# Performance work log

Measured on AMD Instinct MI355X. Metric: run time of the kernel, lower is better.

Reference implementation:

```python
import jax, jax.numpy as jnp
import numpy as np

B, NCH, NPTS, NGT = 8, 4, 1024, 10
NANCH = 5 * NPTS
NMIN, NMAX = 64, 64
M = NMIN + NMAX
NPOOL = 64
EXT = 0.2
EPS = 1e-5
PERM = np.array([3, 4, 5, 1, 0, 2, 6])

_C = jnp.array([[0., 1, 0], [0, -1, 0], [2.5, -1, 0], [2.5, 1, 0], [2.5, 0, 0]], jnp.float32)
_ROT = jnp.array([[1., 0, 0], [0, 0, 1], [0, 1, 0]], jnp.float32)  # theta=0 rotation from source
NEW_CENTERS = _C @ _ROT  # (5,3)
DIM = jnp.array([2., 2., 5.], jnp.float32)


def _conv1x1(x, w, b):
    return jnp.einsum('bci,oc->boi', x, w) + b[None, :, None]


def _bn(x, g, be):  # BatchNorm1d in train mode: batch stats over (N, L)
    m = x.mean((0, 2), keepdims=True)
    v = ((x - m) ** 2).mean((0, 2), keepdims=True)
    return (x - m) * jax.lax.rsqrt(v + EPS) * g[None, :, None] + be[None, :, None]


def _corners(b):  # b=(cx,cz,w,l,ry) -> (4,2) CCW BEV corners
    lx = jnp.array([0.5, -0.5, -0.5, 0.5]) * b[2]
    lz = jnp.array([0.5, 0.5, -0.5, -0.5]) * b[3]
    c, s = jnp.cos(b[4]), jnp.sin(b[4])
    return jnp.stack([b[0] + lx * c - lz * s, b[1] + lx * s + lz * c], 1)


def _clip(poly, count, e1, e2):  # Sutherland-Hodgman: clip convex poly (8,2) by left half-plane of e1->e2
    idx = jnp.arange(8)
    valid = idx < count
    cnt = jnp.maximum(count, 1)
    nxt = poly[(idx + 1) % cnt]
    ex, ez = e2[0] - e1[0], e2[1] - e1[1]
    dc = ex * (poly[:, 1] - e1[1]) - ez * (poly[:, 0] - e1[0])
    dn = ex * (nxt[:, 1] - e1[1]) - ez * (nxt[:, 0] - e1[0])
    in_c, in_n = dc >= 0, dn >= 0
    den = dc - dn
    t = dc / jnp.where(jnp.abs(den) < 1e-9, 1e-9, den)
    inter = poly + t[:, None] * (nxt - poly)
    flags = jnp.stack([valid & in_c, valid & (in_c ^ in_n)], 1).reshape(16)
    pts = jnp.stack([poly, inter], 1).reshape(16, 2)
    pos = jnp.cumsum(flags) - 1
    out = jnp.zeros((8, 2), poly.dtype).at[jnp.where(flags, pos, 8)].set(pts, mode='drop')
    return out, flags.sum()


def _bev_iou(a, b):  # rotated BEV IoU, a,b=(cx,cz,w,l,ry)
    poly = jnp.zeros((8, 2)).at[:4].set(_corners(a))
    count = jnp.int32(4)
    cb = _corners(b)
    for k in range(4):
        poly, count = _clip(poly, count, cb[k], cb[(k + 1) % 4])
    idx = jnp.arange(8)
    nxt = poly[(idx + 1) % jnp.maximum(count, 1)]
    inter = 0.5 * jnp.abs(jnp.sum(jnp.where(idx < count, poly[:, 0] * nxt[:, 1] - nxt[:, 0] * poly[:, 1], 0.)))
    return inter / jnp.maximum(a[2] * a[3] + b[2] * b[3] - inter, 1e-8)


def _bev(b7):  # (..,7)=[x,y,z,h,w,l,ry] -> (cx,cz,w,l,ry)
    return jnp.stack([b7[..., 0], b7[..., 2], b7[..., 4], b7[..., 5], b7[..., 6]], -1)


def _select_one(pnts, labels):  # pnts (N,3), labels (G,9)
    cent = (pnts[:, None, :] - NEW_CENTERS[None]).reshape(NANCH, 3)  # repeat_interleave(pnts,5)-tile(centers)
    anchors = jnp.concatenate([jnp.broadcast_to(DIM, (NANCH, 3)), cent, jnp.zeros((NANCH, 1))], 1)
    a7 = anchors[:, PERM]
    g7 = labels[:, PERM]
    ab, gb = _bev(a7), _bev(g7)
    iou2d = jax.vmap(lambda g: jax.vmap(lambda a: _bev_iou(g, a))(ab))(gb)  # (G, NANCH)
    max_iou = iou2d.max(0)
    max_ind = jnp.argmax(iou2d, 0)
    order = jnp.argsort(max_iou)
    sel = jnp.concatenate([order[:NMIN], order[-NMAX:]])  # bottom-k + top-k
    return a7[sel], max_ind[sel], max_iou[sel]


def _pool_one(box, pts, ft):  # roipool3d: first NPOOL points inside expanded box, zero-padded
    c, s = jnp.cos(box[6]), jnp.sin(box[6])
    dx, dz = pts[:, 0] - box[0], pts[:, 2] - box[2]
    xl = dx * c + dz * s
    zl = -dx * s + dz * c
    inside = (jnp.abs(xl) < box[4] * 0.5 + EXT) & (jnp.abs(zl) < box[5] * 0.5 + EXT) \
             & (pts[:, 1] > box[1] - box[3] - EXT) & (pts[:, 1] < box[1] + EXT)
    order = jnp.argsort(jnp.logical_not(inside))[:NPOOL]  # stable sort: inside points first, original order
    valid = inside[order].astype(ft.dtype)[:, None]
    return jnp.concatenate([ft[order], pts[order]], -1) * valid  # (NPOOL, 256+3)


def _forward(points, gt_labels, p):
    x = jax.nn.relu(_bn(_conv1x1(points, p['pn_w1'], p['pn_b1']), p['pn_g1'], p['pn_be1']))
    x = jax.nn.relu(_bn(_conv1x1(x, p['pn_w2'], p['pn_b2']), p['pn_g2'], p['pn_be2']))
    x = _bn(_conv1x1(x, p['pn_w3'], p['pn_b3']), p['pn_g3'], p['pn_be3'])  # (B,256,N)
    pts = jnp.transpose(points[:, :3, :], (0, 2, 1))  # (B,N,3)
    sel_boxes, sel_idx, sel_iou = jax.vmap(_select_one)(pts, gt_labels)  # (B,M,7),(B,M),(B,M)
    ftr = jnp.transpose(x, (0, 2, 1))  # (B,N,256)
    pooled = jax.vmap(lambda bx, pp, ff: jax.vmap(lambda b: _pool_one(b, pp, ff))(bx))(sel_boxes, pts, ftr)
    pooled = pooled - jnp.pad(sel_boxes[:, :, None, :3], ((0, 0), (0, 0), (0, 0), (256, 0)))  # subtract center from last 3 ch
    pf = jnp.transpose(pooled.reshape(B * M, NPOOL, 259), (0, 2, 1))  # (B*M,259,64)
    f = _bn(_conv1x1(pf, p['rp_w1'], p['rp_b1']), p['rp_g1'], p['rp_be1'])
    f = _bn(_conv1x1(f, p['rp_w2'], p['rp_b2']), p['rp_g2'], p['rp_be2'])
    feats = f.reshape(B, M, 1024, NPOOL).max(-1)
    labels_bin = (sel_iou > 0.5).astype(jnp.int32)
    return feats, labels_bin, sel_iou, sel_boxes, gt_labels[-1], sel_idx


def setup_inputs():
    key = jax.random.key(0)
    ks = jax.random.split(key, 16)
    points = jax.random.normal(ks[0], (B, NCH, NPTS), jnp.float32) * 3.0
    dims = jax.random.uniform(ks[1], (B, NGT, 3), minval=1.0, maxval=4.0)
    ctrs = jax.random.normal(ks[2], (B, NGT, 3)) * 3.0
    th = jax.random.uniform(ks[3], (B, NGT, 1), minval=-3.14, maxval=3.14)
    extra = jax.random.normal(ks[4], (B, NGT, 2))
    gt_labels = jnp.concatenate([dims, ctrs, th, extra], -1).astype(jnp.float32)  # (B,G,9)
    inp = {'points': points, 'gt_labels': gt_labels}
    shapes = [('pn', 1, 64, NCH), ('pn', 2, 128, 64), ('pn', 3, 256, 128), ('rp', 1, 512, 259), ('rp', 2, 1024, 512)]
    for j, (pre, n, o, i) in enumerate(shapes):
        inp[f'{pre}_w{n}'] = jax.random.normal(ks[5 + j], (o, i), jnp.float32) / np.sqrt(i).astype(np.float32)
        inp[f'{pre}_b{n}'] = jnp.zeros((o,), jnp.float32)
        inp[f'{pre}_g{n}'] = jnp.ones((o,), jnp.float32)
        inp[f'{pre}_be{n}'] = jnp.zeros((o,), jnp.float32)
    return inp


def reference(points, gt_labels, pn_w1, pn_b1, pn_g1, pn_be1, pn_w2, pn_b2, pn_g2, pn_be2, pn_w3, pn_b3, pn_g3, pn_be3, rp_w1, rp_b1, rp_g1, rp_be1, rp_w2, rp_b2, rp_g2, rp_be2):
    p = dict(pn_w1=pn_w1, pn_b1=pn_b1, pn_g1=pn_g1, pn_be1=pn_be1, pn_w2=pn_w2, pn_b2=pn_b2, pn_g2=pn_g2, pn_be2=pn_be2, pn_w3=pn_w3, pn_b3=pn_b3, pn_g3=pn_g3, pn_be3=pn_be3, rp_w1=rp_w1, rp_b1=rp_b1, rp_g1=rp_g1, rp_be1=rp_be1, rp_w2=rp_w2, rp_b2=rp_b2, rp_g2=rp_g2, rp_be2=rp_be2)
    return _forward(points, gt_labels, p)
```

## Files before the change

### kernel.cpp

```cpp
#include <hip/hip_runtime.h>
#include <hip/hip_bf16.h>
#include <float.h>
#include <math.h>


typedef __attribute__((ext_vector_type(8))) short short8;
typedef __attribute__((ext_vector_type(4))) float f32x4;

template <int CTRL>
__device__ __forceinline__ float dppmv(float x) {
  return __int_as_float(__builtin_amdgcn_update_dpp(
      0, __float_as_int(x), CTRL, 0xF, 0xF, true));
}
__device__ __forceinline__ float dpp_sum16(float x) {
  x += dppmv<0xB1>(x);
  x += dppmv<0x4E>(x);
  x += dppmv<0x124>(x);
  x += dppmv<0x128>(x);
  return x;
}

__device__ __forceinline__ void stage1k(const unsigned short* g, unsigned short* l) {
  __builtin_amdgcn_global_load_lds(
      (const __attribute__((address_space(1))) unsigned int*)g,
      (__attribute__((address_space(3))) unsigned int*)l, 16, 0, 0);
}

#define FMA16()                                                                 \
  do {                                                                          \
    float4 av = *(const float4*)&sWT[cc][to * 4];                               \
    float4 bv = *(const float4*)&sB[cc][tk * 4];                                \
    acc[0][0] = fmaf(av.x, bv.x, acc[0][0]);                                    \
    acc[0][1] = fmaf(av.x, bv.y, acc[0][1]);                                    \
    acc[0][2] = fmaf(av.x, bv.z, acc[0][2]);                                    \
    acc[0][3] = fmaf(av.x, bv.w, acc[0][3]);                                    \
    acc[1][0] = fmaf(av.y, bv.x, acc[1][0]);                                    \
    acc[1][1] = fmaf(av.y, bv.y, acc[1][1]);                                    \
    acc[1][2] = fmaf(av.y, bv.z, acc[1][2]);                                    \
    acc[1][3] = fmaf(av.y, bv.w, acc[1][3]);                                    \
    acc[2][0] = fmaf(av.z, bv.x, acc[2][0]);                                    \
    acc[2][1] = fmaf(av.z, bv.y, acc[2][1]);                                    \
    acc[2][2] = fmaf(av.z, bv.z, acc[2][2]);                                    \
    acc[2][3] = fmaf(av.z, bv.w, acc[2][3]);                                    \
    acc[3][0] = fmaf(av.w, bv.x, acc[3][0]);                                    \
    acc[3][1] = fmaf(av.w, bv.y, acc[3][1]);                                    \
    acc[3][2] = fmaf(av.w, bv.z, acc[3][2]);                                    \
    acc[3][3] = fmaf(av.w, bv.w, acc[3][3]);                                    \
  } while (0)

template <int C, int O, bool AFF, bool RELU, bool TRANS>
__global__ __launch_bounds__(256) void conv_pn(const float* __restrict__ in,
                                               const float* __restrict__ w,
                                               const float* __restrict__ bias,
                                               const float* __restrict__ aff,
                                               float* __restrict__ out) {
  __shared__ __align__(16) float sB[64][68];
  __shared__ __align__(16) float sWT[64][68];
  const int i0 = blockIdx.x * 64;
  const int o0 = blockIdx.y * 64;
  const int b = blockIdx.z;
  const int tid = threadIdx.x;
  const int tk = tid & 15, to = tid >> 4;
  float acc[4][4] = {};
  for (int c0 = 0; c0 < C; c0 += 64) {
    const int cs = (C - c0 < 64) ? (C - c0) : 64;
    for (int idx = tid; idx < 4096; idx += 256) {
      int ii = idx & 63, cc = idx >> 6;
      float v = 0.f;
      if (cc < cs) {
        int c = c0 + cc;
        v = in[(b * C + c) * 1024 + i0 + ii];
        if (AFF) v = fmaf(v, aff[c], aff[C + c]);
        if (RELU) v = fmaxf(v, 0.f);
      }
      sB[cc][ii] = v;
    }
    for (int idx = tid; idx < 4096; idx += 256) {
      int cc = idx & 63, oo = idx >> 6;
      sWT[cc][oo] = (cc < cs) ? w[(o0 + oo) * C + c0 + cc] : 0.f;
    }
    __syncthreads();
    for (int cc = 0; cc < cs; ++cc) { FMA16(); }
    __syncthreads();
  }
  if (TRANS) {
    float b0 = bias[o0 + to * 4], b1 = bias[o0 + to * 4 + 1];
    float b2 = bias[o0 + to * 4 + 2], b3 = bias[o0 + to * 4 + 3];
#pragma unroll
    for (int jj = 0; jj < 4; ++jj) {
      float4 v = make_float4(acc[0][jj] + b0, acc[1][jj] + b1, acc[2][jj] + b2, acc[3][jj] + b3);
      *(float4*)&out[((size_t)(b * 1024) + i0 + tk * 4 + jj) * O + o0 + to * 4] = v;
    }
  } else {
    for (int j = 0; j < 4; ++j) {
      int o = o0 + to * 4 + j;
      float bs = bias[o];
      float4 v = make_float4(acc[j][0] + bs, acc[j][1] + bs, acc[j][2] + bs, acc[j][3] + bs);
      *(float4*)&out[(b * O + o) * 1024 + i0 + tk * 4] = v;
    }
  }
}

__global__ __launch_bounds__(256) void bn_stats(const float* __restrict__ x,
                                                const float* __restrict__ g,
                                                const float* __restrict__ be,
                                                float* __restrict__ aff, int C) {
#pragma clang fp contract(off)
  int c = blockIdx.x;
  int tid = threadIdx.x;
  float s = 0.f, q = 0.f;
  for (int idx = tid; idx < 8192; idx += 256) {
    int b = idx >> 10, i = idx & 1023;
    float v = x[(b * C + c) * 1024 + i];
    s += v;
    q += v * v;
  }
  for (int m = 1; m < 64; m <<= 1) {
    s += __shfl_xor(s, m);
    q += __shfl_xor(q, m);
  }
  __shared__ float as_[4], aq_[4];
  int wv = tid >> 6;
  if ((tid & 63) == 0) { as_[wv] = s; aq_[wv] = q; }
  __syncthreads();
  if (tid == 0) {
    s = as_[0] + as_[1] + as_[2] + as_[3];
    q = aq_[0] + aq_[1] + aq_[2] + aq_[3];
    float m_ = s * (1.f / 8192.f);
    float var = q * (1.f / 8192.f) - m_ * m_;
    float A = g[c] / sqrtf(var + 1e-5f);
    aff[c] = A;
    aff[C + c] = be[c] - m_ * A;
  }
}

__global__ __launch_bounds__(256) void bn_stats_t(const float* __restrict__ x,
                                                  const float* __restrict__ g,
                                                  const float* __restrict__ be,
                                                  float* __restrict__ aff) {
#pragma clang fp contract(off)
  int c = blockIdx.x;
  int tid = threadIdx.x;
  float s = 0.f, q = 0.f;
  for (int idx = tid; idx < 8192; idx += 256) {
    float v = x[(size_t)idx * 256 + c];
    s += v;
    q += v * v;
  }
  for (int m = 1; m < 64; m <<= 1) {
    s += __shfl_xor(s, m);
    q += __shfl_xor(q, m);
  }
  __shared__ float as_[4], aq_[4];
  int wv = tid >> 6;
  if ((tid & 63) == 0) { as_[wv] = s; aq_[wv] = q; }
  __syncthreads();
  if (tid == 0) {
    s = as_[0] + as_[1] + as_[2] + as_[3];
    q = aq_[0] + aq_[1] + aq_[2] + aq_[3];
    float m_ = s * (1.f / 8192.f);
    float var = q * (1.f / 8192.f) - m_ * m_;
    float A = g[c] / sqrtf(var + 1e-5f);
    aff[c] = A;
    aff[256 + c] = be[c] - m_ * A;
  }
}

__device__ __forceinline__ void poly_ins(float* ox, float* oz, int p, float vx, float vz) {
#pragma unroll
  for (int s = 0; s < 8; ++s)
    if (p == s) { ox[s] = vx; oz[s] = vz; }
}

__device__ float bev_iou_ga(const float* gx, const float* gz, float garea, float ax, float az) {
#pragma clang fp contract(off)
  float px[8], pz[8];
#pragma unroll
  for (int i = 0; i < 4; ++i) {
    px[i] = gx[i];
    pz[i] = gz[i];
    px[i + 4] = 0.f;
    pz[i + 4] = 0.f;
  }
  int count = 4;
  float kx[4], kz[4];
  kx[0] = ax + 1.f;  kz[0] = az + 2.5f;
  kx[1] = ax - 1.f;  kz[1] = az + 2.5f;
  kx[2] = ax - 1.f;  kz[2] = az - 2.5f;
  kx[3] = ax + 1.f;  kz[3] = az - 2.5f;
#pragma unroll
  for (int e = 0; e < 4; ++e) {
    float e1x = kx[e], e1z = kz[e];
    float e2x = kx[(e + 1) & 3], e2z = kz[(e + 1) & 3];
    float ex = e2x - e1x, ez = e2z - e1z;
    int cnt = count > 1 ? count : 1;
    int lim = count < 8 ? count : 8;
    float ox[8] = {}, oz[8] = {};
    int p = 0;
#pragma unroll
    for (int idx = 0; idx < 8; ++idx) {
      if (idx < lim) {
        const int nis = (idx + 1 > 7) ? 7 : idx + 1;
        float nx = px[nis], nz = pz[nis];
        if (idx + 1 == cnt) { nx = px[0]; nz = pz[0]; }
        float cx = px[idx], cz = pz[idx];
        float dc = ex * (cz - e1z) - ez * (cx - e1x);
        float dn = ex * (nz - e1z) - ez * (nx - e1x);
        bool ic = dc >= 0.f, in_ = dn >= 0.f;
        if (ic) {
          poly_ins(ox, oz, p, cx, cz);
          ++p;
        }
        if (ic != in_) {
          float den = dc - dn;
          float t = dc / (fabsf(den) < 1e-9f ? 1e-9f : den);
          poly_ins(ox, oz, p, cx + t * (nx - cx), cz + t * (nz - cz));
          ++p;
        }
      }
    }
    count = p;
    int cp = p < 8 ? p : 8;
#pragma unroll
    for (int i = 0; i < 8; ++i) {
      px[i] = (i < cp) ? ox[i] : 0.f;
      pz[i] = (i < cp) ? oz[i] : 0.f;
    }
  }
  int cnt = count > 1 ? count : 1;
  int lim = count < 8 ? count : 8;
  float ssum = 0.f;
#pragma unroll
  for (int idx = 0; idx < 8; ++idx) {
    if (idx < lim) {
      const int nis = (idx + 1 > 7) ? 7 : idx + 1;
      float nx = px[nis], nz = pz[nis];
      if (idx + 1 == cnt) { nx = px[0]; nz = pz[0]; }
      ssum += px[idx] * nz - nx * pz[idx];
    }
  }
  float inter = 0.5f * fabsf(ssum);
  return inter / fmaxf(garea + 10.f - inter, 1e-8f);
}

__global__ __launch_bounds__(256) void iou_kernel(const float* __restrict__ points,
                                                  const float* __restrict__ gt,
                                                  float* __restrict__ iou10,
                                                  float* __restrict__ o_gt,
                                                  int* __restrict__ rank) {
#pragma clang fp contract(off)
  int b = blockIdx.y, g = blockIdx.z;
  int a = blockIdx.x * 256 + threadIdx.x;
  if (g == 0) rank[b * 5120 + a] = 0;
  if (g == 0 && b == 0 && blockIdx.x == 0 && threadIdx.x < 90)
    o_gt[threadIdx.x] = gt[630 + threadIdx.x];
  const float* L = gt + b * 90 + g * 9;
  float gxx = L[3], gzz = L[5], gw = L[0], gl = L[2], gth = L[6];
  float c = cosf(gth), s = sinf(gth);
  const float sx[4] = {0.5f, -0.5f, -0.5f, 0.5f};
  const float sz[4] = {0.5f, 0.5f, -0.5f, -0.5f};
  float gcx[4], gcz[4];
#pragma unroll
  for (int k = 0; k < 4; ++k) {
    float lx = sx[k] * gw, lz = sz[k] * gl;
    gcx[k] = gxx + lx * c - lz * s;
    gcz[k] = gzz + lx * s + lz * c;
  }
  float garea = gw * gl;
  int pt = a / 5, j = a % 5;
  const float CX[5] = {0.f, 0.f, 2.5f, 2.5f, 2.5f};
  const float CZ[5] = {1.f, -1.f, -1.f, 1.f, 0.f};
  const float* P = points + b * 4096;
  float ax = P[pt] - CX[j];
  float az = P[2048 + pt] - CZ[j];
  iou10[(size_t)(b * 10 + g) * 5120 + a] = bev_iou_ga(gcx, gcz, garea, ax, az);
}

__global__ __launch_bounds__(256) void iou_reduce(const float* __restrict__ iou10,
                                                  float* __restrict__ maxiou,
                                                  int* __restrict__ maxind) {
  int b = blockIdx.y;
  int a = blockIdx.x * 256 + threadIdx.x;
  float best = -1.f;
  int bi = 0;
  for (int g = 0; g < 10; ++g) {
    float v = iou10[(size_t)(b * 10 + g) * 5120 + a];
    if (v > best) { best = v; bi = g; }
  }
  maxiou[b * 5120 + a] = best;
  maxind[b * 5120 + a] = bi;
}

__global__ __launch_bounds__(256) void select_rank(const float* __restrict__ maxiou,
                                                   int* __restrict__ rank) {
  __shared__ __align__(16) float vals[640];
  int b = blockIdx.y, chunk = blockIdx.z, tid = threadIdx.x;
  int jb0 = chunk * 640;
  for (int i = tid; i < 640; i += 256) vals[i] = maxiou[b * 5120 + jb0 + i];
  int a = blockIdx.x * 256 + tid;
  float av = maxiou[b * 5120 + a];
  __syncthreads();
  int rk = 0;
#pragma unroll 4
  for (int j4 = 0; j4 < 160; ++j4) {
    float4 v = *(const float4*)&vals[j4 * 4];
    int jb = jb0 + j4 * 4;
    rk += (v.x < av) || (v.x == av && jb < a);
    rk += (v.y < av) || (v.y == av && jb + 1 < a);
    rk += (v.z < av) || (v.z == av && jb + 2 < a);
    rk += (v.w < av) || (v.w == av && jb + 3 < a);
  }
  atomicAdd(&rank[b * 5120 + a], rk);
}

__global__ __launch_bounds__(256) void select_write(const int* __restrict__ rank,
                                                    const float* __restrict__ maxiou,
                                                    const int* __restrict__ maxind,
                                                    const float* __restrict__ points,
                                                    float* __restrict__ o_lbl,
                                                    float* __restrict__ o_iou,
                                                    float* __restrict__ o_box,
                                                    float* __restrict__ o_idx) {
#pragma clang fp contract(off)
  int b = blockIdx.y, tid = threadIdx.x;
  int a = blockIdx.x * 256 + tid;
  int rk = rank[b * 5120 + a];
  int slot = -1;
  if (rk < 64) slot = rk;
  else if (rk >= 5056) slot = rk - 4992;
  if (slot >= 0) {
    const float CX[5] = {0.f, 0.f, 2.5f, 2.5f, 2.5f};
    const float CZ[5] = {1.f, -1.f, -1.f, 1.f, 0.f};
    int base = b * 128 + slot;
    float av = maxiou[b * 5120 + a];
    o_iou[base] = av;
    o_lbl[base] = av > 0.5f ? 1.f : 0.f;
    o_idx[base] = (float)maxind[b * 5120 + a];
    int pt = a / 5, j = a % 5;
    const float* P = points + b * 4096;
    float* bx = o_box + base * 7;
    bx[0] = P[pt] - CX[j];
    bx[1] = P[1024 + pt];
    bx[2] = P[2048 + pt] - CZ[j];
    bx[3] = 2.f;
    bx[4] = 2.f;
    bx[5] = 5.f;
    bx[6] = 0.f;
  }
}

__global__ __launch_bounds__(256) void pool_kernel(const float* __restrict__ points,
                                                   const float* __restrict__ selboxes,
                                                   int* __restrict__ selpts) {
#pragma clang fp contract(off)
  int box = blockIdx.x * 4 + (threadIdx.x >> 6);
  int lane = threadIdx.x & 63;
  int b = box >> 7;
  const float* bx = selboxes + box * 7;
  float b0 = bx[0], b1 = bx[1], b2 = bx[2], b3 = bx[3], b4 = bx[4], b5 = bx[5];
  float limx = b4 * 0.5f + 0.2f, limz = b5 * 0.5f + 0.2f;
  float ylo = b1 - b3 - 0.2f, yhi = b1 + 0.2f;
  const float* P = points + b * 4096;
  unsigned long long m[16];
  int total_in = 0;
#pragma unroll
  for (int r = 0; r < 16; ++r) {
    int pt = r * 64 + lane;
    float dx = P[pt] - b0;
    float py = P[1024 + pt];
    float dz = P[2048 + pt] - b2;
    bool ins = (fabsf(dx) < limx) && (fabsf(dz) < limz) && (py > ylo) && (py < yhi);
    m[r] = __ballot(ins);
    total_in += __popcll(m[r]);
  }
  unsigned long long lowmask = (1ull << lane) - 1;
  int cum = 0;
#pragma unroll
  for (int r = 0; r < 16; ++r) {
    int pt = r * 64 + lane;
    int inbefore = cum + __popcll(m[r] & lowmask);
    bool ins = (m[r] >> lane) & 1;
    int slot = ins ? inbefore : total_in + (pt - inbefore);
    if (slot < 64) selpts[box * 64 + slot] = pt | (ins ? 0x10000 : 0);
    cum += __popcll(m[r]);
  }
}

__global__ __launch_bounds__(256) void gather_pf(const float* __restrict__ out3T,
                                                 const float* __restrict__ points,
                                                 const int* __restrict__ selpts,
                                                 const float* __restrict__ selboxes,
                                                 const float* __restrict__ aff3,
                                                 unsigned short* __restrict__ pff) {
  __shared__ int sSel[64];
  __shared__ float sCen[3];
  __shared__ float sA3[256], sB3[256];
  const int bm = blockIdx.x;
  const int b = bm >> 7;
  const int tid = threadIdx.x;
  if (tid < 64) sSel[tid] = selpts[bm * 64 + tid];
  if (tid >= 64 && tid < 67) sCen[tid - 64] = selboxes[bm * 7 + (tid - 64)];
  sA3[tid] = aff3[tid];
  sB3[tid] = aff3[256 + tid];
  __syncthreads();
  const int pool = tid >> 2, part = tid & 3;
  const int ni = pool >> 4, nib = pool & 15;
  const int sv = sSel[pool];
  const int pt = sv & 0xFFFF;
  const bool valid = (sv >> 16) != 0;
  const float* row = out3T + ((size_t)(b << 10) + pt) * 256;
#pragma unroll
  for (int ks = 0; ks < 8; ++ks) {
    int c0 = ks * 32 + part * 8;
    float4 x0 = *(const float4*)&row[c0];
    float4 x1 = *(const float4*)&row[c0 + 4];
    float v[8] = {x0.x, x0.y, x0.z, x0.w, x1.x, x1.y, x1.z, x1.w};
    union { __hip_bfloat16 h[8]; uint4 u; } pk;
#pragma unroll
    for (int e = 0; e < 8; ++e) {
      float vv = valid ? fmaf(v[e], sA3[c0 + e], sB3[c0 + e]) : 0.f;
      pk.h[e] = __float2bfloat16(vv);
    }
    *(uint4*)&pff[((size_t)((bm * 9 + ks) * 4 + ni) * 64 + part * 16 + nib) * 8] = pk.u;
  }
  union { __hip_bfloat16 h[8]; uint4 u; } pk;
#pragma unroll
  for (int e = 0; e < 8; ++e) pk.h[e] = __float2bfloat16(0.f);
  if (part == 0) {
#pragma unroll
    for (int d = 0; d < 3; ++d) {
      float pv = valid ? points[(b * 4 + d) * 1024 + pt] : 0.f;
      pk.h[d] = __float2bfloat16(pv - sCen[d]);
    }
  }
  *(uint4*)&pff[((size_t)((bm * 9 + 8) * 4 + ni) * 64 + part * 16 + nib) * 8] = pk.u;
}

__global__ __launch_bounds__(64) void prep_w1(const float* __restrict__ w1,
                                              unsigned short* __restrict__ W1f) {
  int o = blockIdx.x;
  int lp = threadIdx.x;
  if (lp >= 36) return;
  int ks = lp >> 2, quad = lp & 3;
  int tile = o >> 4;
  union { __hip_bfloat16 h[8]; uint4 u; } pk;
#pragma unroll
  for (int j = 0; j < 8; ++j) {
    int c = ks * 32 + quad * 8 + j;
    float v = (c < 259) ? w1[o * 259 + c] : 0.f;
    pk.h[j] = __float2bfloat16(v);
  }
  *(uint4*)&W1f[((size_t)(tile * 9 + ks) * 64 + quad * 16 + (o & 15)) * 8] = pk.u;
}

__global__ __launch_bounds__(256) void rp1_mfma(const unsigned short* __restrict__ W1f,
                                                const unsigned short* __restrict__ pff,
                                                const float* __restrict__ bias1,
                                                unsigned short* __restrict__ g1x,
                                                float* __restrict__ psum4,
                                                float* __restrict__ psq4) {
  __shared__ __align__(16) unsigned short sBuf[2][6144];
  const int tid = threadIdx.x;
  const int lane = tid & 63, w = tid >> 6;
  const int quad = lane >> 4, nib = lane & 15;
  const int l = blockIdx.x;
  const int xcd = l & 7;
  const int j = l >> 3;
  const int ot = j & 3;
  const int bm = xcd * 128 + (j >> 2);
  const unsigned short* Aw = &W1f[((size_t)(ot * 8 + w * 2) * 9 * 64 + lane) * 8];
  const unsigned short* Bg = pff + (size_t)bm * 18432 + w * 1536 + lane * 8;
#pragma unroll
  for (int i = 0; i < 3; ++i)
    stage1k(Bg + i * 512, &sBuf[0][w * 1536 + i * 512]);
  __syncthreads();
  f32x4 acc[2][4] = {};
  int cur = 0;
#pragma unroll
  for (int c = 0; c < 3; ++c) {
    if (c < 2) {
#pragma unroll
      for (int i = 0; i < 3; ++i)
        stage1k(Bg + (c + 1) * 6144 + i * 512, &sBuf[cur ^ 1][w * 1536 + i * 512]);
    }
    const unsigned short* Bl = &sBuf[cur][lane * 8];
#pragma unroll
    for (int k2 = 0; k2 < 3; ++k2) {
      const int ks = c * 3 + k2;
      short8 af[2], bf[4];
#pragma unroll
      for (int mi = 0; mi < 2; ++mi)
        af[mi] = *(const short8*)&Aw[(size_t)(mi * 9 + ks) * 512];
#pragma unroll
      for (int ni = 0; ni < 4; ++ni)
        bf[ni] = *(const short8*)&Bl[(size_t)(k2 * 4 + ni) * 512];
#pragma unroll
      for (int mi = 0; mi < 2; ++mi)
#pragma unroll
        for (int ni = 0; ni < 4; ++ni)
          acc[mi][ni] = __builtin_amdgcn_mfma_f32_16x16x32_bf16(af[mi], bf[ni], acc[mi][ni], 0, 0, 0);
    }
    __syncthreads();
    cur ^= 1;
  }
  const int cbase = ot * 128 + w * 32;
#pragma unroll
  for (int mi = 0; mi < 2; ++mi) {
    float bv[4];
#pragma unroll
    for (int r = 0; r < 4; ++r) bv[r] = bias1[cbase + mi * 16 + quad * 4 + r];
    float s[4] = {0.f, 0.f, 0.f, 0.f}, q[4] = {0.f, 0.f, 0.f, 0.f};
    const int kgbase = (cbase + mi * 16) >> 3;
#pragma unroll
    for (int ni = 0; ni < 4; ++ni) {
      union { __hip_bfloat16 h[4]; unsigned int u[2]; } pk;
#pragma unroll
      for (int r = 0; r < 4; ++r) {
        float v = acc[mi][ni][r] + bv[r];
        pk.h[r] = __float2bfloat16(v);
        s[r] += v;
        q[r] += v * v;
      }
      unsigned int p0 = (unsigned int)__shfl_xor((int)pk.u[0], 16);
      unsigned int p1 = (unsigned int)__shfl_xor((int)pk.u[1], 16);
      if ((quad & 1) == 0) {
        uint4 g = make_uint4(pk.u[0], pk.u[1], p0, p1);
        int kg = kgbase + (quad >> 1);
        *(uint4*)&g1x[((size_t)(bm * 64 + kg) * 64 + ni * 16 + nib) * 8] = g;
      }
    }
#pragma unroll
    for (int r = 0; r < 4; ++r) {
      float ss = dpp_sum16(s[r]);
      float qq = dpp_sum16(q[r]);
      if (nib == 0) {
        int o = cbase + mi * 16 + quad * 4 + r;
        psum4[(size_t)o * 1024 + bm] = ss;
        psq4[(size_t)o * 1024 + bm] = qq;
      }
    }
  }
}

__global__ __launch_bounds__(64) void bn_aff_part(const float* __restrict__ psum,
                                                  const float* __restrict__ psq,
                                                  const float* __restrict__ g,
                                                  const float* __restrict__ be,
                                                  float* __restrict__ aff, int C) {
#pragma clang fp contract(off)
  int o = blockIdx.x;
  int lane = threadIdx.x;
  float s = 0.f, q = 0.f;
  for (int i = 0; i < 16; ++i) {
    int bm = i * 64 + lane;
    s += psum[(size_t)o * 1024 + bm];
    q += psq[(size_t)o * 1024 + bm];
  }
  for (int m = 1; m < 64; m <<= 1) {
    s += __shfl_xor(s, m);
    q += __shfl_xor(q, m);
  }
  if (lane == 0) {
    float m_ = s * (1.f / 65536.f);
    float var = q * (1.f / 65536.f) - m_ * m_;
    float A = g[o] / sqrtf(var + 1e-5f);
    aff[o] = A;
    aff[C + o] = be[o] - m_ * A;
  }
}

__global__ __launch_bounds__(64) void prep_w2(const float* __restrict__ w2,
                                              const float* __restrict__ b2,
                                              const float* __restrict__ aff4,
                                              unsigned short* __restrict__ W2f,
                                              float* __restrict__ bias2p) {
  int o = blockIdx.x;
  int lp = threadIdx.x;
  int ks = lp >> 2, quad = lp & 3;
  int tile = o >> 4;
  float accb = 0.f;
  union { __hip_bfloat16 h[8]; uint4 u; } pk;
#pragma unroll
  for (int j = 0; j < 8; ++j) {
    int c = ks * 32 + quad * 8 + j;
    float wv = w2[o * 512 + c];
    pk.h[j] = __float2bfloat16(wv * aff4[c]);
    accb += wv * aff4[512 + c];
  }
  *(uint4*)&W2f[((size_t)(tile * 16 + ks) * 64 + quad * 16 + (o & 15)) * 8] = pk.u;
  for (int m = 1; m < 64; m <<= 1) accb += __shfl_xor(accb, m);
  if (lp == 0) bias2p[o] = b2[o] + accb;
}

__global__ __launch_bounds__(256) void rp2_mfma(const unsigned short* __restrict__ W2f,
                                                const unsigned short* __restrict__ g1x,
                                                const float* __restrict__ bias2p,
                                                float* __restrict__ maxb,
                                                float* __restrict__ minb,
                                                float* __restrict__ psum,
                                                float* __restrict__ psq) {
  __shared__ __align__(16) unsigned short sBuf[2][8192];
  const int tid = threadIdx.x;
  const int lane = tid & 63, w = tid >> 6;
  const int quad = lane >> 4, nib = lane & 15;
  const int l = blockIdx.x;
  const int xcd = l & 7;
  const int j = l >> 3;
  const int ot = j & 3;
  const int bm = xcd * 128 + (j >> 2);
  const unsigned short* Aw = &W2f[((size_t)(ot * 4 + w) * 4 * 16 * 64 + lane) * 8];
  const unsigned short* Bg = g1x + (size_t)bm * 32768 + w * 2048 + lane * 8;
#pragma unroll
  for (int i = 0; i < 4; ++i)
    stage1k(Bg + i * 512, &sBuf[0][w * 2048 + i * 512]);
  __syncthreads();
  f32x4 acc[4][4] = {};
  int cur = 0;
#pragma unroll
  for (int c = 0; c < 4; ++c) {
    if (c < 3) {
#pragma unroll
      for (int i = 0; i < 4; ++i)
        stage1k(Bg + (c + 1) * 8192 + i * 512, &sBuf[cur ^ 1][w * 2048 + i * 512]);
    }
    const unsigned short* Bl = &sBuf[cur][quad * 512 + nib * 8];
#pragma unroll
    for (int k2 = 0; k2 < 4; ++k2) {
      const int ks = c * 4 + k2;
      short8 af[4], bf[4];
#pragma unroll
      for (int mi = 0; mi < 4; ++mi)
        af[mi] = *(const short8*)&Aw[(size_t)(mi * 16 + ks) * 512];
#pragma unroll
      for (int ni = 0; ni < 4; ++ni)
        bf[ni] = *(const short8*)&Bl[(size_t)(k2 * 2048 + ni * 128)];
#pragma unroll
      for (int mi = 0; mi < 4; ++mi)
#pragma unroll
        for (int ni = 0; ni < 4; ++ni)
          acc[ni][mi] = __builtin_amdgcn_mfma_f32_16x16x32_bf16(bf[ni], af[mi], acc[ni][mi], 0, 0, 0);
    }
    __syncthreads();
    cur ^= 1;
  }
  const int obase = ot * 256 + w * 64;
#pragma unroll
  for (int oi = 0; oi < 4; ++oi) {
    int o = obase + oi * 16 + nib;
    float bs = bias2p[o];
    float mx = -FLT_MAX, mn = FLT_MAX, s = 0.f, q = 0.f;
#pragma unroll
    for (int pi = 0; pi < 4; ++pi) {
#pragma unroll
      for (int r = 0; r < 4; ++r) {
        float v = acc[pi][oi][r] + bs;
        mx = fmaxf(mx, v);
        mn = fminf(mn, v);
        s += v;
        q += v * v;
      }
    }
    mx = fmaxf(mx, __shfl_xor(mx, 16));
    mx = fmaxf(mx, __shfl_xor(mx, 32));
    mn = fminf(mn, __shfl_xor(mn, 16));
    mn = fminf(mn, __shfl_xor(mn, 32));
    s += __shfl_xor(s, 16);
    s += __shfl_xor(s, 32);
    q += __shfl_xor(q, 16);
    q += __shfl_xor(q, 32);
    if (quad == 0) {
      maxb[bm * 1024 + o] = mx;
      minb[bm * 1024 + o] = mn;
      psum[(size_t)o * 1024 + bm] = s;
      psq[(size_t)o * 1024 + bm] = q;
    }
  }
}

__global__ void feats_kernel(const float* __restrict__ maxb, const float* __restrict__ minb,
                             const float* __restrict__ aff5, float* __restrict__ o_feats) {
#pragma clang fp contract(off)
  int i = blockIdx.x * 256 + threadIdx.x;
  int o = i & 1023;
  float A = aff5[o], Bv = aff5[1024 + o];
  float v = (A >= 0.f) ? maxb[i] : minb[i];
  o_feats[i] = v * A + Bv;
}

extern "C" void kernel_launch(void* const* d_in, const int* in_sizes, int n_in,
                              void* d_out, int out_size, void* d_ws, size_t ws_size,
                              hipStream_t stream) {
  (void)in_sizes; (void)n_in; (void)out_size; (void)ws_size;
  const float* points = (const float*)d_in[0];
  const float* gt = (const float*)d_in[1];
  const float* pn_w1 = (const float*)d_in[2];
  const float* pn_b1 = (const float*)d_in[3];
  const float* pn_g1 = (const float*)d_in[4];
  const float* pn_be1 = (const float*)d_in[5];
  const float* pn_w2 = (const float*)d_in[6];
  const float* pn_b2 = (const float*)d_in[7];
  const float* pn_g2 = (const float*)d_in[8];
  const float* pn_be2 = (const float*)d_in[9];
  const float* pn_w3 = (const float*)d_in[10];
  const float* pn_b3 = (const float*)d_in[11];
  const float* pn_g3 = (const float*)d_in[12];
  const float* pn_be3 = (const float*)d_in[13];
  const float* rp_w1 = (const float*)d_in[14];
  const float* rp_b1 = (const float*)d_in[15];
  const float* rp_g1 = (const float*)d_in[16];
  const float* rp_be1 = (const float*)d_in[17];
  const float* rp_w2 = (const float*)d_in[18];
  const float* rp_b2 = (const float*)d_in[19];
  const float* rp_g2 = (const float*)d_in[20];
  const float* rp_be2 = (const float*)d_in[21];

  float* ws = (float*)d_ws;
  float* out1 = ws;
  float* out2 = out1 + 524288;
  float* maxiou = out2 + 1048576;
  int* maxind = (int*)(maxiou + 40960);
  int* selpts = maxind + 40960;
  int* rank = selpts + 65536;
  float* aff1 = (float*)(rank + 40960);
  float* aff2 = aff1 + 128;
  float* aff3 = aff2 + 256;
  float* aff4 = aff3 + 512;
  float* aff5 = aff4 + 1024;
  float* psum4 = aff5 + 2048;
  float* psq4 = psum4 + 524288;
  unsigned short* W1f = (unsigned short*)(psq4 + 524288);
  float* pff_f = (float*)(W1f) + 73728;
  unsigned short* pff = (unsigned short*)pff_f;
  float* g1x_f = pff_f + 9437184;
  unsigned short* g1x = (unsigned short*)g1x_f;
  float* out3T = g1x_f;
  float* iou10 = g1x_f + 2097152;
  float* maxb = pff_f;
  float* minb = maxb + 1048576;
  float* psum5 = minb + 1048576;
  float* psq5 = psum5 + 1048576;
  unsigned short* W2f = (unsigned short*)out1;
  float* bias2p = out1 + 262144;

  float* o_feats = (float*)d_out;
  float* o_lbl = o_feats + 1048576;
  float* o_iou = o_lbl + 1024;
  float* o_box = o_iou + 1024;
  float* o_gt = o_box + 7168;
  float* o_idx = o_gt + 90;

  conv_pn<4, 64, false, false, false><<<dim3(16, 1, 8), 256, 0, stream>>>(points, pn_w1, pn_b1, nullptr, out1);
  bn_stats<<<64, 256, 0, stream>>>(out1, pn_g1, pn_be1, aff1, 64);
  conv_pn<64, 128, true, true, false><<<dim3(16, 2, 8), 256, 0, stream>>>(out1, pn_w2, pn_b2, aff1, out2);
  bn_stats<<<128, 256, 0, stream>>>(out2, pn_g2, pn_be2, aff2, 128);
  conv_pn<128, 256, true, true, true><<<dim3(16, 4, 8), 256, 0, stream>>>(out2, pn_w3, pn_b3, aff2, out3T);
  bn_stats_t<<<256, 256, 0, stream>>>(out3T, pn_g3, pn_be3, aff3);
  iou_kernel<<<dim3(20, 8, 10), 256, 0, stream>>>(points, gt, iou10, o_gt, rank);
  iou_reduce<<<dim3(20, 8), 256, 0, stream>>>(iou10, maxiou, maxind);
  select_rank<<<dim3(20, 8, 8), 256, 0, stream>>>(maxiou, rank);
  select_write<<<dim3(20, 8), 256, 0, stream>>>(rank, maxiou, maxind, points, o_lbl, o_iou, o_box, o_idx);
  pool_kernel<<<256, 256, 0, stream>>>(points, o_box, selpts);
  gather_pf<<<1024, 256, 0, stream>>>(out3T, points, selpts, o_box, aff3, pff);
  prep_w1<<<512, 64, 0, stream>>>(rp_w1, W1f);
  rp1_mfma<<<4096, 256, 0, stream>>>(W1f, pff, rp_b1, g1x, psum4, psq4);
  bn_aff_part<<<512, 64, 0, stream>>>(psum4, psq4, rp_g1, rp_be1, aff4, 512);
  prep_w2<<<1024, 64, 0, stream>>>(rp_w2, rp_b2, aff4, W2f, bias2p);
  rp2_mfma<<<4096, 256, 0, stream>>>(W2f, g1x, bias2p, maxb, minb, psum5, psq5);
  bn_aff_part<<<1024, 64, 0, stream>>>(psum5, psq5, rp_g2, rp_be2, aff5, 1024);
  feats_kernel<<<4096, 256, 0, stream>>>(maxb, minb, aff5, o_feats);
}
```

Before: 364.5 us.

## Merge pn conv3, IoU computation and W1 prep into one heterogeneous launch

```diff
diff --git a/kernel.cpp b/kernel.cpp
--- a/kernel.cpp
+++ b/kernel.cpp
@@ -243,37 +243,94 @@
   return inter / fmaxf(garea + 10.f - inter, 1e-8f);
 }
 
-__global__ __launch_bounds__(256) void iou_kernel(const float* __restrict__ points,
-                                                  const float* __restrict__ gt,
-                                                  float* __restrict__ iou10,
-                                                  float* __restrict__ o_gt,
-                                                  int* __restrict__ rank) {
+__global__ __launch_bounds__(256) void fused_mid(
+    const float* __restrict__ in2, const float* __restrict__ w3,
+    const float* __restrict__ b3, const float* __restrict__ aff2,
+    float* __restrict__ out3T,
+    const float* __restrict__ points, const float* __restrict__ gt,
+    float* __restrict__ iou10, float* __restrict__ o_gt, int* __restrict__ rank,
+    const float* __restrict__ w1, unsigned short* __restrict__ W1f) {
+  __shared__ __align__(16) float sB[64][68];
+  __shared__ __align__(16) float sWT[64][68];
+  const int bid = blockIdx.x;
+  const int tid = threadIdx.x;
+  if (bid < 512) {
+    const int i0 = (bid & 15) * 64;
+    const int o0 = ((bid >> 4) & 3) * 64;
+    const int b = bid >> 6;
+    const int tk = tid & 15, to = tid >> 4;
+    float acc[4][4] = {};
+    for (int c0 = 0; c0 < 128; c0 += 64) {
+      for (int idx = tid; idx < 4096; idx += 256) {
+        int ii = idx & 63, cc = idx >> 6;
+        int c = c0 + cc;
+        float v = in2[(b * 128 + c) * 1024 + i0 + ii];
+        v = fmaf(v, aff2[c], aff2[128 + c]);
+        v = fmaxf(v, 0.f);
+        sB[cc][ii] = v;
+      }
+      for (int idx = tid; idx < 4096; idx += 256) {
+        int cc = idx & 63, oo = idx >> 6;
+        sWT[cc][oo] = w3[(o0 + oo) * 128 + c0 + cc];
+      }
+      __syncthreads();
+      for (int cc = 0; cc < 64; ++cc) { FMA16(); }
+      __syncthreads();
+    }
+    float c0v = b3[o0 + to * 4], c1v = b3[o0 + to * 4 + 1];
+    float c2v = b3[o0 + to * 4 + 2], c3v = b3[o0 + to * 4 + 3];
+#pragma unroll
+    for (int jj = 0; jj < 4; ++jj) {
+      float4 v = make_float4(acc[0][jj] + c0v, acc[1][jj] + c1v, acc[2][jj] + c2v, acc[3][jj] + c3v);
+      *(float4*)&out3T[((size_t)(b * 1024) + i0 + tk * 4 + jj) * 256 + o0 + to * 4] = v;
+    }
+  } else if (bid < 2112) {
 #pragma clang fp contract(off)
-  int b = blockIdx.y, g = blockIdx.z;
-  int a = blockIdx.x * 256 + threadIdx.x;
-  if (g == 0) rank[b * 5120 + a] = 0;
-  if (g == 0 && b == 0 && blockIdx.x == 0 && threadIdx.x < 90)
-    o_gt[threadIdx.x] = gt[630 + threadIdx.x];
-  const float* L = gt + b * 90 + g * 9;
-  float gxx = L[3], gzz = L[5], gw = L[0], gl = L[2], gth = L[6];
-  float c = cosf(gth), s = sinf(gth);
-  const float sx[4] = {0.5f, -0.5f, -0.5f, 0.5f};
-  const float sz[4] = {0.5f, 0.5f, -0.5f, -0.5f};
-  float gcx[4], gcz[4];
-#pragma unroll
-  for (int k = 0; k < 4; ++k) {
-    float lx = sx[k] * gw, lz = sz[k] * gl;
-    gcx[k] = gxx + lx * c - lz * s;
-    gcz[k] = gzz + lx * s + lz * c;
-  }
-  float garea = gw * gl;
-  int pt = a / 5, j = a % 5;
-  const float CX[5] = {0.f, 0.f, 2.5f, 2.5f, 2.5f};
-  const float CZ[5] = {1.f, -1.f, -1.f, 1.f, 0.f};
-  const float* P = points + b * 4096;
-  float ax = P[pt] - CX[j];
-  float az = P[2048 + pt] - CZ[j];
-  iou10[(size_t)(b * 10 + g) * 5120 + a] = bev_iou_ga(gcx, gcz, garea, ax, az);
+    int r = bid - 512;
+    int g = r / 160;
+    int rb = r % 160;
+    int b = rb / 20;
+    int axb = rb % 20;
+    int a = axb * 256 + tid;
+    if (g == 0) rank[b * 5120 + a] = 0;
+    if (g == 0 && b == 0 && axb == 0 && tid < 90)
+      o_gt[tid] = gt[630 + tid];
+    const float* L = gt + b * 90 + g * 9;
+    float gxx = L[3], gzz = L[5], gw = L[0], gl = L[2], gth = L[6];
+    float c = cosf(gth), s = sinf(gth);
+    const float sx[4] = {0.5f, -0.5f, -0.5f, 0.5f};
+    const float sz[4] = {0.5f, 0.5f, -0.5f, -0.5f};
+    float gcx[4], gcz[4];
+#pragma unroll
+    for (int k = 0; k < 4; ++k) {
+      float lx = sx[k] * gw, lz = sz[k] * gl;
+      gcx[k] = gxx + lx * c - lz * s;
+      gcz[k] = gzz + lx * s + lz * c;
+    }
+    float garea = gw * gl;
+    int pt = a / 5, j = a % 5;
+    const float CX[5] = {0.f, 0.f, 2.5f, 2.5f, 2.5f};
+    const float CZ[5] = {1.f, -1.f, -1.f, 1.f, 0.f};
+    const float* P = points + b * 4096;
+    float ax = P[pt] - CX[j];
+    float az = P[2048 + pt] - CZ[j];
+    iou10[(size_t)(b * 10 + g) * 5120 + a] = bev_iou_ga(gcx, gcz, garea, ax, az);
+  } else {
+    int o = (bid - 2112) * 4 + (tid >> 6);
+    int lp = tid & 63;
+    if (lp < 36) {
+      int ks = lp >> 2, quad = lp & 3;
+      int tile = o >> 4;
+      union { __hip_bfloat16 h[8]; uint4 u; } pk;
+#pragma unroll
+      for (int j = 0; j < 8; ++j) {
+        int c = ks * 32 + quad * 8 + j;
+        float v = (c < 259) ? w1[o * 259 + c] : 0.f;
+        pk.h[j] = __float2bfloat16(v);
+      }
+      *(uint4*)&W1f[((size_t)(tile * 9 + ks) * 64 + quad * 16 + (o & 15)) * 8] = pk.u;
+    }
+  }
 }
 
 __global__ __launch_bounds__(256) void iou_reduce(const float* __restrict__ iou10,
@@ -436,23 +493,6 @@
   *(uint4*)&pff[((size_t)((bm * 9 + 8) * 4 + ni) * 64 + part * 16 + nib) * 8] = pk.u;
 }
 
-__global__ __launch_bounds__(64) void prep_w1(const float* __restrict__ w1,
-                                              unsigned short* __restrict__ W1f) {
-  int o = blockIdx.x;
-  int lp = threadIdx.x;
-  if (lp >= 36) return;
-  int ks = lp >> 2, quad = lp & 3;
-  int tile = o >> 4;
-  union { __hip_bfloat16 h[8]; uint4 u; } pk;
-#pragma unroll
-  for (int j = 0; j < 8; ++j) {
-    int c = ks * 32 + quad * 8 + j;
-    float v = (c < 259) ? w1[o * 259 + c] : 0.f;
-    pk.h[j] = __float2bfloat16(v);
-  }
-  *(uint4*)&W1f[((size_t)(tile * 9 + ks) * 64 + quad * 16 + (o & 15)) * 8] = pk.u;
-}
-
 __global__ __launch_bounds__(256) void rp1_mfma(const unsigned short* __restrict__ W1f,
                                                 const unsigned short* __restrict__ pff,
                                                 const float* __restrict__ bias1,
@@ -753,15 +793,15 @@
   bn_stats<<<64, 256, 0, stream>>>(out1, pn_g1, pn_be1, aff1, 64);
   conv_pn<64, 128, true, true, false><<<dim3(16, 2, 8), 256, 0, stream>>>(out1, pn_w2, pn_b2, aff1, out2);
   bn_stats<<<128, 256, 0, stream>>>(out2, pn_g2, pn_be2, aff2, 128);
-  conv_pn<128, 256, true, true, true><<<dim3(16, 4, 8), 256, 0, stream>>>(out2, pn_w3, pn_b3, aff2, out3T);
+  fused_mid<<<2240, 256, 0, stream>>>(out2, pn_w3, pn_b3, aff2, out3T,
+                                      points, gt, iou10, o_gt, rank,
+                                      rp_w1, W1f);
   bn_stats_t<<<256, 256, 0, stream>>>(out3T, pn_g3, pn_be3, aff3);
-  iou_kernel<<<dim3(20, 8, 10), 256, 0, stream>>>(points, gt, iou10, o_gt, rank);
   iou_reduce<<<dim3(20, 8), 256, 0, stream>>>(iou10, maxiou, maxind);
   select_rank<<<dim3(20, 8, 8), 256, 0, stream>>>(maxiou, rank);
   select_write<<<dim3(20, 8), 256, 0, stream>>>(rank, maxiou, maxind, points, o_lbl, o_iou, o_box, o_idx);
   pool_kernel<<<256, 256, 0, stream>>>(points, o_box, selpts);
   gather_pf<<<1024, 256, 0, stream>>>(out3T, points, selpts, o_box, aff3, pff);
-  prep_w1<<<512, 64, 0, stream>>>(rp_w1, W1f);
   rp1_mfma<<<4096, 256, 0, stream>>>(W1f, pff, rp_b1, g1x, psum4, psq4);
   bn_aff_part<<<512, 64, 0, stream>>>(psum4, psq4, rp_g1, rp_be1, aff4, 512);
   prep_w2<<<1024, 64, 0, stream>>>(rp_w2, rp_b2, aff4, W2f, bias2p);
```

Result: faster. 352.0 us (-3.4%).
